# Optimization experiments

Measured on AMD Instinct MI355X. Metric: run time of the kernel, lower is better.

## Reference

```python
import jax, jax.numpy as jnp
import numpy as np

# Graph sizes: each graph has exactly 32 nodes (forced by the rearrange + lin1 in_features)
BS = 4096
NODES = 32
N = BS * NODES          # 131072 total nodes
F_IN = 128
E_PER_G = 512
E = BS * E_PER_G        # 2097152 edges, all within-graph
HID = 1024
NCLS = 10


def setup_inputs() -> dict:
    key = jax.random.key(0)
    ks = jax.random.split(key, 9)
    x = jax.random.normal(ks[0], (N, F_IN), dtype=jnp.float32)
    # within-graph random edges: local node ids in [0,32) + per-graph offset
    graph_off = jnp.repeat(jnp.arange(BS, dtype=jnp.int64), E_PER_G) * NODES
    src = jax.random.randint(ks[1], (E,), 0, NODES, dtype=jnp.int64) + graph_off
    dst = jax.random.randint(ks[2], (E,), 0, NODES, dtype=jnp.int64) + graph_off
    edge_index = jnp.stack([src, dst], axis=0)
    s = 0.05
    gconv_w = jax.random.normal(ks[3], (F_IN, F_IN), dtype=jnp.float32) * s
    gconv_b = jax.random.normal(ks[4], (F_IN,), dtype=jnp.float32) * s
    lin1_w = jax.random.normal(ks[5], (HID, F_IN * NODES), dtype=jnp.float32) * s
    lin1_b = jax.random.normal(ks[6], (HID,), dtype=jnp.float32) * s
    lin2_w = jax.random.normal(ks[7], (NCLS, HID), dtype=jnp.float32) * s
    lin2_b = jax.random.normal(ks[8], (NCLS,), dtype=jnp.float32) * s
    return {"x": x, "edge_index": edge_index, "gconv_w": gconv_w,
            "gconv_b": gconv_b, "lin1_w": lin1_w, "lin1_b": lin1_b,
            "lin2_w": lin2_w, "lin2_b": lin2_b, "bs": BS}


def reference(x, edge_index, gconv_w, gconv_b, lin1_w, lin1_b, lin2_w, lin2_b, bs):
    # GINConv (eps=0): h_i = Linear( x_i + sum_{j->i} x_j )
    src, dst = edge_index[0], edge_index[1]
    agg = jax.ops.segment_sum(x[src], dst, num_segments=x.shape[0])  # [N, F]
    h = (x + agg) @ gconv_w.T + gconv_b                               # [N, F]
    h = jax.nn.relu(h)
    # rearrange '(bs e) f -> bs (f e)' with e=32 nodes per graph
    f = h.shape[-1]
    h = h.reshape(bs, NODES, f).transpose(0, 2, 1).reshape(bs, f * NODES)
    h = h @ lin1_w.T + lin1_b
    # dropout is identity in eval mode
    h = jax.nn.relu(h)
    h = h @ lin2_w.T + lin2_b
    return jax.nn.softmax(h, axis=-1)
```

## Files before the change

### kernel.cpp

```cpp
#include <hip/hip_runtime.h>

typedef _Float16 half_t;
typedef _Float16 halfv8 __attribute__((ext_vector_type(8)));
typedef _Float16 halfv4 __attribute__((ext_vector_type(4)));
typedef float    floatv4 __attribute__((ext_vector_type(4)));
typedef unsigned int uint;
typedef uint uintv4 __attribute__((ext_vector_type(4)));

#define NODES 32
#define FIN   128
#define EPG   512
#define NBS   4096
#define ETOT  (NBS*EPG)
#define HID   1024
#define KDIM  4096
#define NCLS  10
#define YPITCH 36

#define BM 256
#define BN 256
#define BK 64
#define KS 4
#define KSLEN (KDIM/KS)
#define NT (KSLEN/BK)

#define GLDS16(g, l)                                                        \
  __builtin_amdgcn_global_load_lds(                                         \
      (const __attribute__((address_space(1))) unsigned int*)(g),           \
      (__attribute__((address_space(3))) unsigned int*)(l), 16, 0, 0)

__global__ __launch_bounds__(256) void prep_w1(const float* __restrict__ w1,
                                               half_t* __restrict__ w1p,
                                               const float* __restrict__ gw,
                                               half_t* __restrict__ gw16) {
  __shared__ float tmp[FIN * 33];
  const int o = blockIdx.x, t = threadIdx.x;
  if (t < 16) {
    const int i = o * 16 + t;
    gw16[i] = (half_t)gw[i];
  }
  const floatv4* src = (const floatv4*)(w1 + (size_t)o * KDIM);
  for (int i = t; i < KDIM / 4; i += 256) {
    floatv4 v = src[i];
    const int f = i >> 3;
    const int n = (i & 7) * 4;
#pragma unroll
    for (int q = 0; q < 4; ++q) tmp[f * 33 + n + q] = v[q];
  }
  __syncthreads();
  half_t* dst = w1p + (size_t)o * KDIM;
  for (int i = t; i < KDIM; i += 256) {
    const int n = i >> 7, f = i & 127;
    dst[i] = (half_t)tmp[f * 33 + n];
  }
}

__global__ __launch_bounds__(256, 3) void gin_fused(
    const float* __restrict__ x, const int* __restrict__ ei,
    const half_t* __restrict__ gw16, const float* __restrict__ gb,
    half_t* __restrict__ H) {
  __shared__ __attribute__((aligned(16))) half_t Yt[4][FIN * YPITCH];
  __shared__ __attribute__((aligned(16))) uint  cnt[4][512];

  const int t = threadIdx.x, w = t >> 6, l = t & 63;
  const int lr = l & 15, lk = l >> 4;
  const int g = blockIdx.x * 4 + w;

  const float* xg = x + (size_t)g * (NODES * FIN);
  floatv4 xr[2][4][2];
#pragma unroll
  for (int mt = 0; mt < 2; ++mt)
#pragma unroll
    for (int kk = 0; kk < 4; ++kk) {
      const float* p = xg + (mt * 16 + lr) * FIN + kk * 32 + lk * 8;
      xr[mt][kk][0] = *(const floatv4*)p;
      xr[mt][kk][1] = *(const floatv4*)(p + 4);
    }
  const int* sp = ei + (size_t)g * EPG;
  const int* dp = ei + (size_t)ETOT + (size_t)g * EPG;
  uintv4 s0 = *(const uintv4*)(sp + l * 8);
  uintv4 s1 = *(const uintv4*)(sp + l * 8 + 4);
  uintv4 d0 = *(const uintv4*)(dp + l * 8);
  uintv4 d1 = *(const uintv4*)(dp + l * 8 + 4);

  {
    uintv4* c4 = (uintv4*)cnt[w];
    uintv4 z = {0, 0, 0, 0};
    c4[l] = z;
    c4[l + 64] = z;
  }
#pragma unroll
  for (int q = 0; q < 4; ++q) {
    uint p0 = (d0[q] & 31) * 32 + (s0[q] & 31);
    atomicAdd(&cnt[w][p0 >> 1], 1u << ((p0 & 1) * 16));
    uint p1 = (d1[q] & 31) * 32 + (s1[q] & 31);
    atomicAdd(&cnt[w][p1 >> 1], 1u << ((p1 & 1) * 16));
  }

  halfv8 af[2][4];
#pragma unroll
  for (int mt = 0; mt < 2; ++mt)
#pragma unroll
    for (int kk = 0; kk < 4; ++kk) {
      halfv8 h;
#pragma unroll
      for (int q = 0; q < 4; ++q) {
        h[q]     = (half_t)xr[mt][kk][0][q];
        h[q + 4] = (half_t)xr[mt][kk][1][q];
      }
      af[mt][kk] = h;
    }

  floatv4 acc[2][8] = {};
#pragma unroll
  for (int kk = 0; kk < 4; ++kk) {
    halfv8 bfk[8];
#pragma unroll
    for (int nt = 0; nt < 8; ++nt)
      bfk[nt] = *(const halfv8*)(gw16 + (nt * 16 + lr) * FIN + kk * 32 + lk * 8);
#pragma unroll
    for (int nt = 0; nt < 8; ++nt)
#pragma unroll
      for (int mt = 0; mt < 2; ++mt)
        acc[mt][nt] = __builtin_amdgcn_mfma_f32_16x16x32_f16(af[mt][kk], bfk[nt],
                                                             acc[mt][nt], 0, 0, 0);
  }

  half_t* yw = Yt[w];
#pragma unroll
  for (int mt = 0; mt < 2; ++mt)
#pragma unroll
    for (int nt = 0; nt < 8; ++nt) {
      halfv4 h = {(half_t)acc[mt][nt][0], (half_t)acc[mt][nt][1],
                  (half_t)acc[mt][nt][2], (half_t)acc[mt][nt][3]};
      *(halfv4*)&yw[(nt * 16 + lr) * YPITCH + mt * 16 + lk * 4] = h;
    }

  const unsigned short* c16 = (const unsigned short*)cnt[w];
  halfv8 am[2];
#pragma unroll
  for (int mt = 0; mt < 2; ++mt) {
    const int i = mt * 16 + lr;
#pragma unroll
    for (int q = 0; q < 8; ++q) {
      const int j = lk * 8 + q;
      float c = (float)c16[i * 32 + j] + ((j == i) ? 1.f : 0.f);
      am[mt][q] = (half_t)c;
    }
  }

  floatv4 acc2[2][8] = {};
#pragma unroll
  for (int nt = 0; nt < 8; ++nt) {
    halfv8 bf = *(const halfv8*)&yw[(nt * 16 + lr) * YPITCH + lk * 8];
#pragma unroll
    for (int mt = 0; mt < 2; ++mt)
      acc2[mt][nt] = __builtin_amdgcn_mfma_f32_16x16x32_f16(am[mt], bf,
                                                            acc2[mt][nt], 0, 0, 0);
  }

  half_t* Hg = H + (size_t)g * KDIM;
#pragma unroll
  for (int nt = 0; nt < 8; ++nt) {
    const float bias = gb[nt * 16 + lr];
#pragma unroll
    for (int mt = 0; mt < 2; ++mt)
#pragma unroll
      for (int q = 0; q < 4; ++q) {
        const int m = mt * 16 + lk * 4 + q;
        const float v = acc2[mt][nt][q] + bias;
        Hg[m * FIN + nt * 16 + lr] = (half_t)(v > 0.f ? v : 0.f);
      }
  }
}

__global__ __launch_bounds__(512, 2) void lin1_gemm(
    const half_t* __restrict__ A, const half_t* __restrict__ B,
    half_t* __restrict__ Cbase) {
  __shared__ __attribute__((aligned(16))) half_t As[2][BM * BK];
  __shared__ __attribute__((aligned(16))) half_t Bs[2][BN * BK];

  const int t = threadIdx.x;
  const int orig = blockIdx.x;
  const int wg = (orig & 7) * 32 + (orig >> 3);
  const int mt = wg & 15, rest = wg >> 4;
  const int nt_ = rest & 3, ks = rest >> 2;
  const int m0 = mt * BM, n0 = nt_ * BN, k0 = ks * KSLEN;

  const half_t* gA[4];
  const half_t* gB[4];
#pragma unroll
  for (int j = 0; j < 4; ++j) {
    const int L = t + j * 512;
    const int r = L >> 3;
    const int c = (L & 7) ^ (r & 7);
    gA[j] = A + (size_t)(m0 + r) * KDIM + k0 + c * 8;
    gB[j] = B + (size_t)(n0 + r) * KDIM + k0 + c * 8;
  }

#define STAGE(buf, koff)                                                    \
  {                                                                         \
    _Pragma("unroll")                                                       \
    for (int j = 0; j < 4; ++j)                                             \
      GLDS16(gA[j] + (koff), &As[buf][(t + j * 512) * 8]);                  \
    _Pragma("unroll")                                                       \
    for (int j = 0; j < 4; ++j)                                             \
      GLDS16(gB[j] + (koff), &Bs[buf][(t + j * 512) * 8]);                  \
  }

  const int w = t >> 6, l = t & 63, lr = l & 15, lk = l >> 4;
  const int wm = (w >> 2) * 128, wn = (w & 3) * 64;

  floatv4 acc[8][4] = {};

  STAGE(0, 0)
  STAGE(1, BK)
  asm volatile("s_waitcnt vmcnt(8)" ::: "memory");
  __builtin_amdgcn_s_barrier();

  for (int kt = 0; kt < NT; ++kt) {
    const int cur = kt & 1;
    const half_t* as = As[cur];
    const half_t* bs = Bs[cur];
#pragma unroll
    for (int ksb = 0; ksb < 2; ++ksb) {
      halfv8 bf[4], af[8];
#pragma unroll
      for (int nf = 0; nf < 4; ++nf) {
        const int row = wn + nf * 16 + lr;
        const int ch = (ksb * 4 + lk) ^ (row & 7);
        bf[nf] = *(const halfv8*)&bs[row * BK + ch * 8];
      }
#pragma unroll
      for (int mf = 0; mf < 8; ++mf) {
        const int row = wm + mf * 16 + lr;
        const int ch = (ksb * 4 + lk) ^ (row & 7);
        af[mf] = *(const halfv8*)&as[row * BK + ch * 8];
      }
      __builtin_amdgcn_s_setprio(1);
#pragma unroll
      for (int mf = 0; mf < 8; ++mf)
#pragma unroll
        for (int nf = 0; nf < 4; ++nf)
          acc[mf][nf] = __builtin_amdgcn_mfma_f32_16x16x32_f16(
              af[mf], bf[nf], acc[mf][nf], 0, 0, 0);
      __builtin_amdgcn_s_setprio(0);
    }
    __builtin_amdgcn_s_barrier();
    const int src = (kt + 2 < NT) ? (kt + 2) : 0;
    STAGE(cur, src * BK)
    asm volatile("s_waitcnt vmcnt(8)" ::: "memory");
    __builtin_amdgcn_s_barrier();
  }

  half_t* C = Cbase + (size_t)ks * ((size_t)NBS * HID);
#pragma unroll
  for (int mf = 0; mf < 8; ++mf)
#pragma unroll
    for (int nf = 0; nf < 4; ++nf) {
      const int n = n0 + wn + nf * 16 + lr;
#pragma unroll
      for (int q = 0; q < 4; ++q) {
        const int m = m0 + wm + mf * 16 + lk * 4 + q;
        C[(size_t)m * HID + n] = (half_t)acc[mf][nf][q];
      }
    }
#undef STAGE
}

__global__ __launch_bounds__(256) void head(
    const half_t* __restrict__ Cb, const float* __restrict__ b1,
    const float* __restrict__ w2, const float* __restrict__ b2,
    float* __restrict__ out) {
  __shared__ __attribute__((aligned(16))) float w2s[NCLS * HID];
  const int t = threadIdx.x;
  {
    const floatv4* s4 = (const floatv4*)w2;
    floatv4* d4 = (floatv4*)w2s;
    for (int i = t; i < (NCLS * HID) / 4; i += 256) d4[i] = s4[i];
  }
  __syncthreads();
  const int w = t >> 6, l = t & 63;
  const int row = blockIdx.x * 4 + w;

  float r[16];
#pragma unroll
  for (int jj = 0; jj < 4; ++jj) {
    floatv4 bb = *(const floatv4*)&b1[jj * 256 + l * 4];
    float s[4] = {bb[0], bb[1], bb[2], bb[3]};
#pragma unroll
    for (int p = 0; p < KS; ++p) {
      const half_t* cp = Cb + (size_t)p * ((size_t)NBS * HID) + (size_t)row * HID;
      halfv4 u = *(const halfv4*)&cp[jj * 256 + l * 4];
#pragma unroll
      for (int q = 0; q < 4; ++q) s[q] += (float)u[q];
    }
#pragma unroll
    for (int q = 0; q < 4; ++q) r[jj * 4 + q] = s[q] > 0.f ? s[q] : 0.f;
  }
  float lg[10];
#pragma unroll
  for (int c = 0; c < NCLS; ++c) {
    float p = 0.f;
#pragma unroll
    for (int jj = 0; jj < 4; ++jj) {
      floatv4 wv = *(const floatv4*)&w2s[c * HID + jj * 256 + l * 4];
      p += r[jj * 4 + 0] * wv[0] + r[jj * 4 + 1] * wv[1] +
           r[jj * 4 + 2] * wv[2] + r[jj * 4 + 3] * wv[3];
    }
#pragma unroll
    for (int off = 32; off >= 1; off >>= 1) p += __shfl_xor(p, off);
    lg[c] = p + b2[c];
  }
  float mx = lg[0];
#pragma unroll
  for (int c = 1; c < NCLS; ++c) mx = fmaxf(mx, lg[c]);
  float sum = 0.f;
#pragma unroll
  for (int c = 0; c < NCLS; ++c) { lg[c] = __expf(lg[c] - mx); sum += lg[c]; }
  const float inv = 1.f / sum;
  float myv = 0.f;
#pragma unroll
  for (int c = 0; c < NCLS; ++c) myv = (l == c) ? lg[c] * inv : myv;
  if (l < NCLS) out[(size_t)row * NCLS + l] = myv;
}

extern "C" void kernel_launch(void* const* d_in, const int* in_sizes, int n_in,
                              void* d_out, int out_size, void* d_ws, size_t ws_size,
                              hipStream_t stream) {
  (void)in_sizes; (void)n_in; (void)out_size; (void)ws_size;
  const float* x  = (const float*)d_in[0];
  const int*   ei = (const int*)d_in[1];
  const float* gw = (const float*)d_in[2];
  const float* gb = (const float*)d_in[3];
  const float* w1 = (const float*)d_in[4];
  const float* b1 = (const float*)d_in[5];
  const float* w2 = (const float*)d_in[6];
  const float* b2 = (const float*)d_in[7];
  float* out = (float*)d_out;

  char* ws = (char*)d_ws;
  half_t* H    = (half_t*)(ws);
  half_t* w1p  = (half_t*)(ws + 33554432);
  half_t* C    = (half_t*)(ws + 33554432 + 8388608);
  half_t* gw16 = (half_t*)(ws + 33554432 + 8388608 + (size_t)KS * NBS * HID * 2);

  prep_w1  <<<dim3(HID),     dim3(256), 0, stream>>>(w1, w1p, gw, gw16);
  gin_fused<<<dim3(NBS / 4), dim3(256), 0, stream>>>(x, ei, gw16, gb, H);
  lin1_gemm<<<dim3(16 * 4 * KS), dim3(512), 0, stream>>>(H, w1p, C);
  head     <<<dim3(NBS / 4), dim3(256), 0, stream>>>(C, b1, w2, b2, out);
}
```

Baseline: 94.97 us.

## Split GIN into feature GEMM plus mixing kernel and re-pipeline lin1 GEMM

The fused GIN kernel is split in two. One kernel computes x·Wᵀ for all nodes and writes it transposed to a workspace buffer. The second builds the per-graph adjacency counts and applies them by MFMA, reading its B fragments straight from global memory instead of going through LDS. The lin1 GEMM now stages 32-wide K halves into a finer LDS layout with a 4-phase schedule that interleaves loads with MFMA, aiming for better overlap and less LDS use. This adds a kernel launch and an extra round trip of the intermediate through global memory, and the C buffer now shares workspace with Zt.

```diff
diff --git a/kernel.cpp b/kernel.cpp
--- a/kernel.cpp
+++ b/kernel.cpp
@@ -12,10 +12,10 @@
 #define EPG   512
 #define NBS   4096
 #define ETOT  (NBS*EPG)
+#define NTOT  (NBS*NODES)
 #define HID   1024
 #define KDIM  4096
 #define NCLS  10
-#define YPITCH 36
 
 #define BM 256
 #define BN 256
@@ -55,34 +55,64 @@
   }
 }
 
-__global__ __launch_bounds__(256, 3) void gin_fused(
-    const float* __restrict__ x, const int* __restrict__ ei,
-    const half_t* __restrict__ gw16, const float* __restrict__ gb,
-    half_t* __restrict__ H) {
-  __shared__ __attribute__((aligned(16))) half_t Yt[4][FIN * YPITCH];
-  __shared__ __attribute__((aligned(16))) uint  cnt[4][512];
-
+__global__ __launch_bounds__(256, 3) void zw_gemm(
+    const float* __restrict__ x, const half_t* __restrict__ gw16,
+    half_t* __restrict__ Zt) {
+  const int t = threadIdx.x, w = t >> 6, l = t & 63;
+  const int lr = l & 15, lk = l >> 4;
+  const size_t base = (size_t)blockIdx.x * 64 + w * 16;
+
+  const float* xp = x + (base + lr) * FIN;
+  floatv4 xq[8];
+#pragma unroll
+  for (int kk = 0; kk < 4; ++kk) {
+    xq[kk * 2]     = *(const floatv4*)(xp + kk * 32 + lk * 8);
+    xq[kk * 2 + 1] = *(const floatv4*)(xp + kk * 32 + lk * 8 + 4);
+  }
+  floatv4 acc[8] = {};
+#pragma unroll
+  for (int kk = 0; kk < 4; ++kk) {
+    halfv8 af;
+#pragma unroll
+    for (int q = 0; q < 4; ++q) {
+      af[q]     = (half_t)xq[kk * 2][q];
+      af[q + 4] = (half_t)xq[kk * 2 + 1][q];
+    }
+    halfv8 bf[8];
+#pragma unroll
+    for (int nt = 0; nt < 8; ++nt)
+      bf[nt] = *(const halfv8*)(gw16 + (nt * 16 + lr) * FIN + kk * 32 + lk * 8);
+#pragma unroll
+    for (int nt = 0; nt < 8; ++nt)
+      acc[nt] = __builtin_amdgcn_mfma_f32_16x16x32_f16(af, bf[nt], acc[nt], 0, 0, 0);
+  }
+#pragma unroll
+  for (int nt = 0; nt < 8; ++nt) {
+    halfv4 h = {(half_t)acc[nt][0], (half_t)acc[nt][1],
+                (half_t)acc[nt][2], (half_t)acc[nt][3]};
+    *(halfv4*)(Zt + (size_t)(nt * 16 + lr) * NTOT + base + lk * 4) = h;
+  }
+}
+
+__global__ __launch_bounds__(256, 3) void gin_mix(
+    const half_t* __restrict__ Zt, const int* __restrict__ ei,
+    const float* __restrict__ gb, half_t* __restrict__ H) {
+  __shared__ uint cnt[4][512];
   const int t = threadIdx.x, w = t >> 6, l = t & 63;
   const int lr = l & 15, lk = l >> 4;
   const int g = blockIdx.x * 4 + w;
 
-  const float* xg = x + (size_t)g * (NODES * FIN);
-  floatv4 xr[2][4][2];
-#pragma unroll
-  for (int mt = 0; mt < 2; ++mt)
-#pragma unroll
-    for (int kk = 0; kk < 4; ++kk) {
-      const float* p = xg + (mt * 16 + lr) * FIN + kk * 32 + lk * 8;
-      xr[mt][kk][0] = *(const floatv4*)p;
-      xr[mt][kk][1] = *(const floatv4*)(p + 4);
-    }
+  halfv8 bf[8];
+#pragma unroll
+  for (int nt = 0; nt < 8; ++nt)
+    bf[nt] = *(const halfv8*)(Zt + (size_t)(nt * 16 + lr) * NTOT +
+                              (size_t)g * 32 + lk * 8);
   const int* sp = ei + (size_t)g * EPG;
   const int* dp = ei + (size_t)ETOT + (size_t)g * EPG;
   uintv4 s0 = *(const uintv4*)(sp + l * 8);
   uintv4 s1 = *(const uintv4*)(sp + l * 8 + 4);
   uintv4 d0 = *(const uintv4*)(dp + l * 8);
   uintv4 d1 = *(const uintv4*)(dp + l * 8 + 4);
-
   {
     uintv4* c4 = (uintv4*)cnt[w];
     uintv4 z = {0, 0, 0, 0};
@@ -96,46 +126,6 @@
     uint p1 = (d1[q] & 31) * 32 + (s1[q] & 31);
     atomicAdd(&cnt[w][p1 >> 1], 1u << ((p1 & 1) * 16));
   }
-
-  halfv8 af[2][4];
-#pragma unroll
-  for (int mt = 0; mt < 2; ++mt)
-#pragma unroll
-    for (int kk = 0; kk < 4; ++kk) {
-      halfv8 h;
-#pragma unroll
-      for (int q = 0; q < 4; ++q) {
-        h[q]     = (half_t)xr[mt][kk][0][q];
-        h[q + 4] = (half_t)xr[mt][kk][1][q];
-      }
-      af[mt][kk] = h;
-    }
-
-  floatv4 acc[2][8] = {};
-#pragma unroll
-  for (int kk = 0; kk < 4; ++kk) {
-    halfv8 bfk[8];
-#pragma unroll
-    for (int nt = 0; nt < 8; ++nt)
-      bfk[nt] = *(const halfv8*)(gw16 + (nt * 16 + lr) * FIN + kk * 32 + lk * 8);
-#pragma unroll
-    for (int nt = 0; nt < 8; ++nt)
-#pragma unroll
-      for (int mt = 0; mt < 2; ++mt)
-        acc[mt][nt] = __builtin_amdgcn_mfma_f32_16x16x32_f16(af[mt][kk], bfk[nt],
-                                                             acc[mt][nt], 0, 0, 0);
-  }
-
-  half_t* yw = Yt[w];
-#pragma unroll
-  for (int mt = 0; mt < 2; ++mt)
-#pragma unroll
-    for (int nt = 0; nt < 8; ++nt) {
-      halfv4 h = {(half_t)acc[mt][nt][0], (half_t)acc[mt][nt][1],
-                  (half_t)acc[mt][nt][2], (half_t)acc[mt][nt][3]};
-      *(halfv4*)&yw[(nt * 16 + lr) * YPITCH + mt * 16 + lk * 4] = h;
-    }
-
   const unsigned short* c16 = (const unsigned short*)cnt[w];
   halfv8 am[2];
 #pragma unroll
@@ -148,17 +138,13 @@
       am[mt][q] = (half_t)c;
     }
   }
-
   floatv4 acc2[2][8] = {};
 #pragma unroll
-  for (int nt = 0; nt < 8; ++nt) {
-    halfv8 bf = *(const halfv8*)&yw[(nt * 16 + lr) * YPITCH + lk * 8];
+  for (int nt = 0; nt < 8; ++nt)
 #pragma unroll
     for (int mt = 0; mt < 2; ++mt)
-      acc2[mt][nt] = __builtin_amdgcn_mfma_f32_16x16x32_f16(am[mt], bf,
+      acc2[mt][nt] = __builtin_amdgcn_mfma_f32_16x16x32_f16(am[mt], bf[nt],
                                                             acc2[mt][nt], 0, 0, 0);
-  }
-
   half_t* Hg = H + (size_t)g * KDIM;
 #pragma unroll
   for (int nt = 0; nt < 8; ++nt) {
@@ -177,8 +163,8 @@
 __global__ __launch_bounds__(512, 2) void lin1_gemm(
     const half_t* __restrict__ A, const half_t* __restrict__ B,
     half_t* __restrict__ Cbase) {
-  __shared__ __attribute__((aligned(16))) half_t As[2][BM * BK];
-  __shared__ __attribute__((aligned(16))) half_t Bs[2][BN * BK];
+  __shared__ __attribute__((aligned(16))) half_t As[2 * 2 * 256 * 32];
+  __shared__ __attribute__((aligned(16))) half_t Bs[2 * 2 * 256 * 32];
 
   const int t = threadIdx.x;
   const int orig = blockIdx.x;
@@ -187,70 +173,94 @@
   const int nt_ = rest & 3, ks = rest >> 2;
   const int m0 = mt * BM, n0 = nt_ * BN, k0 = ks * KSLEN;
 
-  const half_t* gA[4];
-  const half_t* gB[4];
-#pragma unroll
-  for (int j = 0; j < 4; ++j) {
-    const int L = t + j * 512;
-    const int r = L >> 3;
-    const int c = (L & 7) ^ (r & 7);
-    gA[j] = A + (size_t)(m0 + r) * KDIM + k0 + c * 8;
-    gB[j] = B + (size_t)(n0 + r) * KDIM + k0 + c * 8;
-  }
-
-#define STAGE(buf, koff)                                                    \
-  {                                                                         \
-    _Pragma("unroll")                                                       \
-    for (int j = 0; j < 4; ++j)                                             \
-      GLDS16(gA[j] + (koff), &As[buf][(t + j * 512) * 8]);                  \
-    _Pragma("unroll")                                                       \
-    for (int j = 0; j < 4; ++j)                                             \
-      GLDS16(gB[j] + (koff), &Bs[buf][(t + j * 512) * 8]);                  \
-  }
+  const int L0 = t, L1 = t + 512;
+  const int r0 = L0 >> 2, c0 = (L0 & 3) ^ (r0 & 3);
+  const int r1 = L1 >> 2, c1 = (L1 & 3) ^ (r1 & 3);
+  const half_t* srcA0 = A + (size_t)(m0 + r0) * KDIM + k0 + c0 * 8;
+  const half_t* srcA1 = A + (size_t)(m0 + r1) * KDIM + k0 + c1 * 8;
+  const half_t* srcB0 = B + (size_t)(n0 + r0) * KDIM + k0 + c0 * 8;
+  const half_t* srcB1 = B + (size_t)(n0 + r1) * KDIM + k0 + c1 * 8;
+
+#define STAGE_A(buf, kh, tt)                                                  \
+  { GLDS16(srcA0 + (tt) * BK + (kh) * 32, &As[(buf) * 16384 + (kh) * 8192 + L0 * 8]); \
+    GLDS16(srcA1 + (tt) * BK + (kh) * 32, &As[(buf) * 16384 + (kh) * 8192 + L1 * 8]); }
+#define STAGE_B(buf, kh, tt)                                                  \
+  { GLDS16(srcB0 + (tt) * BK + (kh) * 32, &Bs[(buf) * 16384 + (kh) * 8192 + L0 * 8]); \
+    GLDS16(srcB1 + (tt) * BK + (kh) * 32, &Bs[(buf) * 16384 + (kh) * 8192 + L1 * 8]); }
 
   const int w = t >> 6, l = t & 63, lr = l & 15, lk = l >> 4;
   const int wm = (w >> 2) * 128, wn = (w & 3) * 64;
 
   floatv4 acc[8][4] = {};
 
-  STAGE(0, 0)
-  STAGE(1, BK)
-  asm volatile("s_waitcnt vmcnt(8)" ::: "memory");
-  __builtin_amdgcn_s_barrier();
+  STAGE_A(0, 0, 0) STAGE_B(0, 0, 0) STAGE_A(0, 1, 0) STAGE_B(0, 1, 0)
+
+#define PHASE(cur, mh, kh, DO_WAIT, STAGE_STMT)                               \
+  {                                                                           \
+    if (DO_WAIT) asm volatile("s_waitcnt vmcnt(4)" ::: "memory");             \
+    __builtin_amdgcn_s_barrier();                                             \
+    __builtin_amdgcn_sched_barrier(0);                                        \
+    halfv8 af[4], bf[4];                                                      \
+    _Pragma("unroll")                                                         \
+    for (int nf = 0; nf < 4; ++nf) {                                          \
+      const int row = wn + nf * 16 + lr;                                      \
+      bf[nf] = *(const halfv8*)&Bs[(cur) * 16384 + (kh) * 8192 + row * 32 +   \
+                                   ((lk ^ (row & 3)) * 8)];                   \
+    }                                                                         \
+    _Pragma("unroll")                                                         \
+    for (int mf = 0; mf < 4; ++mf) {                                          \
+      const int row = wm + (mh) * 64 + mf * 16 + lr;                          \
+      af[mf] = *(const halfv8*)&As[(cur) * 16384 + (kh) * 8192 + (row & 127) * 32 + \
+                                   ((lk ^ (row & 3)) * 8)];                   \
+    }                                                                         \
+    STAGE_STMT;                                                               \
+    __builtin_amdgcn_s_setprio(1);                                            \
+    _Pragma("unroll")                                                         \
+    for (int mf = 0; mf < 4; ++mf)                                            \
+      _Pragma("unroll")                                                       \
+      for (int nf = 0; nf < 4; ++nf)                                          \
+        acc[(mh) * 4 + mf][nf] = __builtin_amdgcn_mfma_f32_16x16x32_f16(      \
+            af[mf], bf[nf], acc[(mh) * 4 + mf][nf], 0, 0, 0);                 \
+    __builtin_amdgcn_s_setprio(0);                                            \
+  }
+
+#undef PHASE
+#define PHASE(cur, mh, kh, DO_WAIT, STAGE_STMT)                               \
+  {                                                                           \
+    if (DO_WAIT) asm volatile("s_waitcnt vmcnt(4)" ::: "memory");             \
+    __builtin_amdgcn_s_barrier();                                             \
+    __builtin_amdgcn_sched_barrier(0);                                        \
+    halfv8 af[4], bf[4];                                                      \
+    _Pragma("unroll")                                                         \
+    for (int nf = 0; nf < 4; ++nf) {                                          \
+      const int row = wn + nf * 16 + lr;                                      \
+      bf[nf] = *(const halfv8*)&Bs[(cur) * 16384 + (kh) * 8192 + row * 32 +   \
+                                   ((lk ^ (row & 3)) * 8)];                   \
+    }                                                                         \
+    _Pragma("unroll")                                                         \
+    for (int mf = 0; mf < 4; ++mf) {                                          \
+      const int row = wm + (mh) * 64 + mf * 16 + lr;                          \
+      af[mf] = *(const halfv8*)&As[(cur) * 16384 + (kh) * 8192 + row * 32 +   \
+                                   ((lk ^ (row & 3)) * 8)];                   \
+    }                                                                         \
+    STAGE_STMT;                                                               \
+    __builtin_amdgcn_s_setprio(1);                                            \
+    _Pragma("unroll")                                                         \
+    for (int mf = 0; mf < 4; ++mf)                                            \
+      _Pragma("unroll")                                                       \
+      for (int nf = 0; nf < 4; ++nf)                                          \
+        acc[(mh) * 4 + mf][nf] = __builtin_amdgcn_mfma_f32_16x16x32_f16(      \
+            af[mf], bf[nf], acc[(mh) * 4 + mf][nf], 0, 0, 0);                 \
+    __builtin_amdgcn_s_setprio(0);                                            \
+  }
 
   for (int kt = 0; kt < NT; ++kt) {
-    const int cur = kt & 1;
-    const half_t* as = As[cur];
-    const half_t* bs = Bs[cur];
-#pragma unroll
-    for (int ksb = 0; ksb < 2; ++ksb) {
-      halfv8 bf[4], af[8];
-#pragma unroll
-      for (int nf = 0; nf < 4; ++nf) {
-        const int row = wn + nf * 16 + lr;
-        const int ch = (ksb * 4 + lk) ^ (row & 7);
-        bf[nf] = *(const halfv8*)&bs[row * BK + ch * 8];
-      }
-#pragma unroll
-      for (int mf = 0; mf < 8; ++mf) {
-        const int row = wm + mf * 16 + lr;
-        const int ch = (ksb * 4 + lk) ^ (row & 7);
-        af[mf] = *(const halfv8*)&as[row * BK + ch * 8];
-      }
-      __builtin_amdgcn_s_setprio(1);
-#pragma unroll
-      for (int mf = 0; mf < 8; ++mf)
-#pragma unroll
-        for (int nf = 0; nf < 4; ++nf)
-          acc[mf][nf] = __builtin_amdgcn_mfma_f32_16x16x32_f16(
-              af[mf], bf[nf], acc[mf][nf], 0, 0, 0);
-      __builtin_amdgcn_s_setprio(0);
-    }
-    __builtin_amdgcn_s_barrier();
-    const int src = (kt + 2 < NT) ? (kt + 2) : 0;
-    STAGE(cur, src * BK)
-    asm volatile("s_waitcnt vmcnt(8)" ::: "memory");
-    __builtin_amdgcn_s_barrier();
+    const int cur = kt & 1, nxt = cur ^ 1;
+    const int ttn = (kt + 1 < NT) ? (kt + 1) : 0;
+    PHASE(cur, 0, 0, 1, STAGE_A(nxt, 0, ttn))
+    PHASE(cur, 1, 0, 0, STAGE_B(nxt, 0, ttn))
+    PHASE(cur, 0, 1, 1, STAGE_A(nxt, 1, ttn))
+    PHASE(cur, 1, 1, 0, STAGE_B(nxt, 1, ttn))
   }
 
   half_t* C = Cbase + (size_t)ks * ((size_t)NBS * HID);
@@ -265,7 +275,9 @@
         C[(size_t)m * HID + n] = (half_t)acc[mf][nf][q];
       }
     }
-#undef STAGE
+#undef PHASE
+#undef STAGE_A
+#undef STAGE_B
 }
 
 __global__ __launch_bounds__(256) void head(
@@ -340,13 +352,15 @@
   float* out = (float*)d_out;
 
   char* ws = (char*)d_ws;
-  half_t* H    = (half_t*)(ws);
-  half_t* w1p  = (half_t*)(ws + 33554432);
-  half_t* C    = (half_t*)(ws + 33554432 + 8388608);
-  half_t* gw16 = (half_t*)(ws + 33554432 + 8388608 + (size_t)KS * NBS * HID * 2);
-
-  prep_w1  <<<dim3(HID),     dim3(256), 0, stream>>>(w1, w1p, gw, gw16);
-  gin_fused<<<dim3(NBS / 4), dim3(256), 0, stream>>>(x, ei, gw16, gb, H);
-  lin1_gemm<<<dim3(16 * 4 * KS), dim3(512), 0, stream>>>(H, w1p, C);
-  head     <<<dim3(NBS / 4), dim3(256), 0, stream>>>(C, b1, w2, b2, out);
-}
+  half_t* Zt   = (half_t*)(ws);
+  half_t* C    = (half_t*)(ws);
+  half_t* H    = (half_t*)(ws + 33554432);
+  half_t* w1p  = (half_t*)(ws + 67108864);
+  half_t* gw16 = (half_t*)(ws + 75497472);
+
+  prep_w1  <<<dim3(HID),      dim3(256), 0, stream>>>(w1, w1p, gw, gw16);
+  zw_gemm  <<<dim3(NTOT/64),  dim3(256), 0, stream>>>(x, gw16, Zt);
+  gin_mix  <<<dim3(NBS/4),    dim3(256), 0, stream>>>(Zt, ei, gb, H);
+  lin1_gemm<<<dim3(16*4*KS),  dim3(512), 0, stream>>>(H, w1p, C);
+  head     <<<dim3(NBS/4),    dim3(256), 0, stream>>>(C, b1, w2, b2, out);
+}
```

Measured after the change: 121.6 us. +28.0%, slower.

## Store GIN output feature-major, drop w1 transpose, stage x via LDS loads

Applied to the files above, without the earlier changes.

The weight prep kernel no longer transposes lin1 weights through shared memory. It becomes a flat fp32-to-fp16 conversion of w1 and the GIN weights together. To match, gin_fused now writes H in feature-major order, which is the natural w1 column order. It first stages the tile in LDS and then does coalesced 16-byte global stores, instead of scattered 2-byte stores. x is loaded with swizzled global_load_lds into a shared buffer that is reused for Y and the output. Occupancy drops to 2 blocks per CU because each block now uses more LDS.

```diff
diff --git a/kernel.cpp b/kernel.cpp
--- a/kernel.cpp
+++ b/kernel.cpp
@@ -15,7 +15,7 @@
 #define HID   1024
 #define KDIM  4096
 #define NCLS  10
-#define YPITCH 36
+#define YP    36
 
 #define BM 256
 #define BN 256
@@ -29,53 +29,42 @@
       (const __attribute__((address_space(1))) unsigned int*)(g),           \
       (__attribute__((address_space(3))) unsigned int*)(l), 16, 0, 0)
 
-__global__ __launch_bounds__(256) void prep_w1(const float* __restrict__ w1,
-                                               half_t* __restrict__ w1p,
-                                               const float* __restrict__ gw,
-                                               half_t* __restrict__ gw16) {
-  __shared__ float tmp[FIN * 33];
-  const int o = blockIdx.x, t = threadIdx.x;
-  if (t < 16) {
-    const int i = o * 16 + t;
-    gw16[i] = (half_t)gw[i];
-  }
-  const floatv4* src = (const floatv4*)(w1 + (size_t)o * KDIM);
-  for (int i = t; i < KDIM / 4; i += 256) {
-    floatv4 v = src[i];
-    const int f = i >> 3;
-    const int n = (i & 7) * 4;
-#pragma unroll
-    for (int q = 0; q < 4; ++q) tmp[f * 33 + n + q] = v[q];
-  }
-  __syncthreads();
-  half_t* dst = w1p + (size_t)o * KDIM;
-  for (int i = t; i < KDIM; i += 256) {
-    const int n = i >> 7, f = i & 127;
-    dst[i] = (half_t)tmp[f * 33 + n];
-  }
-}
-
-__global__ __launch_bounds__(256, 3) void gin_fused(
+__global__ __launch_bounds__(256) void prep_cvt(const float* __restrict__ w1,
+                                                half_t* __restrict__ w1p,
+                                                const float* __restrict__ gw,
+                                                half_t* __restrict__ gw16) {
+  const size_t q = (size_t)blockIdx.x * 256 + threadIdx.x;
+  const float* s;
+  half_t* d;
+  size_t off;
+  if (q < 1048576) { s = w1; d = w1p; off = q; }
+  else             { s = gw; d = gw16; off = q - 1048576; }
+  floatv4 v = *(const floatv4*)(s + off * 4);
+  halfv4 h = {(half_t)v[0], (half_t)v[1], (half_t)v[2], (half_t)v[3]};
+  *(halfv4*)(d + off * 4) = h;
+}
+
+__global__ __launch_bounds__(256, 2) void gin_fused(
     const float* __restrict__ x, const int* __restrict__ ei,
     const half_t* __restrict__ gw16, const float* __restrict__ gb,
     half_t* __restrict__ H) {
-  __shared__ __attribute__((aligned(16))) half_t Yt[4][FIN * YPITCH];
-  __shared__ __attribute__((aligned(16))) uint  cnt[4][512];
+  __shared__ __attribute__((aligned(16))) half_t buf[4][8192];
+  __shared__ uint cnt[4][512];
 
   const int t = threadIdx.x, w = t >> 6, l = t & 63;
   const int lr = l & 15, lk = l >> 4;
   const int g = blockIdx.x * 4 + w;
-
   const float* xg = x + (size_t)g * (NODES * FIN);
-  floatv4 xr[2][4][2];
-#pragma unroll
-  for (int mt = 0; mt < 2; ++mt)
-#pragma unroll
-    for (int kk = 0; kk < 4; ++kk) {
-      const float* p = xg + (mt * 16 + lr) * FIN + kk * 32 + lk * 8;
-      xr[mt][kk][0] = *(const floatv4*)p;
-      xr[mt][kk][1] = *(const floatv4*)(p + 4);
-    }
+  half_t* bw = buf[w];
+
+#pragma unroll
+  for (int i = 0; i < 16; ++i) {
+    const int p = i * 64 + l;
+    const int r = p >> 5, c = p & 31;
+    const int cs = (c & ~7) | ((c & 7) ^ (r & 7));
+    GLDS16(xg + r * FIN + cs * 4, bw + (size_t)p * 8);
+  }
+
   const int* sp = ei + (size_t)g * EPG;
   const int* dp = ei + (size_t)ETOT + (size_t)g * EPG;
   uintv4 s0 = *(const uintv4*)(sp + l * 8);
@@ -97,16 +86,22 @@
     atomicAdd(&cnt[w][p1 >> 1], 1u << ((p1 & 1) * 16));
   }
 
+  asm volatile("s_waitcnt vmcnt(0)" ::: "memory");
   halfv8 af[2][4];
 #pragma unroll
   for (int mt = 0; mt < 2; ++mt)
 #pragma unroll
     for (int kk = 0; kk < 4; ++kk) {
+      const int rr = mt * 16 + lr;
+      const int c0 = kk * 8 + ((lk * 2 + 0) ^ (lr & 7));
+      const int c1 = kk * 8 + ((lk * 2 + 1) ^ (lr & 7));
+      floatv4 u = *(const floatv4*)&bw[(rr * 32 + c0) * 8];
+      floatv4 v = *(const floatv4*)&bw[(rr * 32 + c1) * 8];
       halfv8 h;
 #pragma unroll
       for (int q = 0; q < 4; ++q) {
-        h[q]     = (half_t)xr[mt][kk][0][q];
-        h[q + 4] = (half_t)xr[mt][kk][1][q];
+        h[q]     = (half_t)u[q];
+        h[q + 4] = (half_t)v[q];
       }
       af[mt][kk] = h;
     }
@@ -125,15 +120,15 @@
         acc[mt][nt] = __builtin_amdgcn_mfma_f32_16x16x32_f16(af[mt][kk], bfk[nt],
                                                              acc[mt][nt], 0, 0, 0);
   }
-
-  half_t* yw = Yt[w];
+  __builtin_amdgcn_sched_barrier(0);
+
 #pragma unroll
   for (int mt = 0; mt < 2; ++mt)
 #pragma unroll
     for (int nt = 0; nt < 8; ++nt) {
       halfv4 h = {(half_t)acc[mt][nt][0], (half_t)acc[mt][nt][1],
                   (half_t)acc[mt][nt][2], (half_t)acc[mt][nt][3]};
-      *(halfv4*)&yw[(nt * 16 + lr) * YPITCH + mt * 16 + lk * 4] = h;
+      *(halfv4*)&bw[(nt * 16 + lr) * YP + mt * 16 + lk * 4] = h;
     }
 
   const unsigned short* c16 = (const unsigned short*)cnt[w];
@@ -152,25 +147,37 @@
   floatv4 acc2[2][8] = {};
 #pragma unroll
   for (int nt = 0; nt < 8; ++nt) {
-    halfv8 bf = *(const halfv8*)&yw[(nt * 16 + lr) * YPITCH + lk * 8];
+    halfv8 bf = *(const halfv8*)&bw[(nt * 16 + lr) * YP + lk * 8];
 #pragma unroll
     for (int mt = 0; mt < 2; ++mt)
       acc2[mt][nt] = __builtin_amdgcn_mfma_f32_16x16x32_f16(am[mt], bf,
                                                             acc2[mt][nt], 0, 0, 0);
   }
-
-  half_t* Hg = H + (size_t)g * KDIM;
+  __builtin_amdgcn_sched_barrier(0);
+
 #pragma unroll
   for (int nt = 0; nt < 8; ++nt) {
     const float bias = gb[nt * 16 + lr];
 #pragma unroll
-    for (int mt = 0; mt < 2; ++mt)
+    for (int mt = 0; mt < 2; ++mt) {
+      halfv4 h;
 #pragma unroll
       for (int q = 0; q < 4; ++q) {
-        const int m = mt * 16 + lk * 4 + q;
         const float v = acc2[mt][nt][q] + bias;
-        Hg[m * FIN + nt * 16 + lr] = (half_t)(v > 0.f ? v : 0.f);
-      }
+        h[q] = (half_t)(v > 0.f ? v : 0.f);
+      }
+      *(halfv4*)&bw[(nt * 16 + lr) * YP + mt * 16 + lk * 4] = h;
+    }
+  }
+  __builtin_amdgcn_sched_barrier(0);
+
+  half_t* Hg = H + (size_t)g * KDIM;
+#pragma unroll
+  for (int c = 0; c < 8; ++c) {
+    const int ch = c * 64 + l;
+    const int o = ch >> 2, m0 = (ch & 3) * 8;
+    halfv8 v = *(const halfv8*)&bw[o * YP + m0];
+    *(halfv8*)(Hg + ch * 8) = v;
   }
 }
 
@@ -341,11 +348,11 @@
 
   char* ws = (char*)d_ws;
   half_t* H    = (half_t*)(ws);
-  half_t* w1p  = (half_t*)(ws + 33554432);
-  half_t* C    = (half_t*)(ws + 33554432 + 8388608);
-  half_t* gw16 = (half_t*)(ws + 33554432 + 8388608 + (size_t)KS * NBS * HID * 2);
-
-  prep_w1  <<<dim3(HID),     dim3(256), 0, stream>>>(w1, w1p, gw, gw16);
+  half_t* C    = (half_t*)(ws + 33554432);
+  half_t* w1p  = (half_t*)(ws + 67108864);
+  half_t* gw16 = (half_t*)(ws + 75497472);
+
+  prep_cvt <<<dim3(4112),    dim3(256), 0, stream>>>(w1, w1p, gw, gw16);
   gin_fused<<<dim3(NBS / 4), dim3(256), 0, stream>>>(x, ei, gw16, gb, H);
   lin1_gemm<<<dim3(16 * 4 * KS), dim3(512), 0, stream>>>(H, w1p, C);
   head     <<<dim3(NBS / 4), dim3(256), 0, stream>>>(C, b1, w2, b2, out);
```

After: 96.86 us. Within noise of the previous version (+2.0%).
